# Kernel tuning notes

Hardware: AMD Instinct MI355X
Metric: run time of the kernel (lower is better)

Reference implementation:

```python
import jax, jax.numpy as jnp
import numpy as np

L, B, S, H = 2, 32, 2048, 512


def setup_inputs() -> dict:
    key = jax.random.key(0)
    k0, k1, k2, k3, k4 = jax.random.split(key, 5)
    scale = 1.0 / np.sqrt(H).astype(np.float32)  # ~PyTorch LSTMCell init scale
    return {
        "X": jax.random.normal(k0, (B, S, H), jnp.float32),
        "W_ih": jax.random.normal(k1, (L, 4 * H, H), jnp.float32) * scale,
        "W_hh": jax.random.normal(k2, (L, 4 * H, H), jnp.float32) * scale,
        "b_ih": jax.random.normal(k3, (L, 4 * H), jnp.float32) * scale,
        "b_hh": jax.random.normal(k4, (L, 4 * H), jnp.float32) * scale,
    }


def _lstm_layer(x, Wih, Whh, bih, bhh):
    # x: [S, B, I]; gate order matches torch.nn.LSTMCell: i, f, g, o
    Bb = x.shape[1]
    Hh = Whh.shape[1]
    h0 = jnp.zeros((Bb, Hh), x.dtype)
    c0 = jnp.zeros((Bb, Hh), x.dtype)
    # precompute input contribution for all timesteps: [S, B, 4H]
    xg = jnp.einsum('sbi,gi->sbg', x, Wih) + bih + bhh

    def step(carry, xg_t):
        h, c = carry
        gates = xg_t + h @ Whh.T  # [B, 4H]
        i, f, g, o = jnp.split(gates, 4, axis=-1)
        c = jax.nn.sigmoid(f) * c + jax.nn.sigmoid(i) * jnp.tanh(g)
        h = jax.nn.sigmoid(o) * jnp.tanh(c)
        return (h, c), h

    (hT, cT), hs = jax.lax.scan(step, (h0, c0), xg)
    return hs, hT, cT  # hs: [S, B, H]


def reference(X, W_ih, W_hh, b_ih, b_hh):
    # eval mode: variational dropout (dropout_i = dropout_h = 0) is identity;
    # no residual, no reverse.
    x = jnp.transpose(X, (1, 0, 2))  # [S, B, I]
    n_layers = W_ih.shape[0]
    hT = cT = None
    for l in range(n_layers):
        x, hT, cT = _lstm_layer(x, W_ih[l], W_hh[l], b_ih[l], b_hh[l])
    ht = jnp.transpose(x, (1, 0, 2))  # [B, S, H]
    # states = (ht[:, -1], ct[:, -1]) of final layer
    return ht, hT, cT
```

## Files before the change

kernel.cpp:

```cpp
#include <hip/hip_runtime.h>

typedef unsigned short u16;
typedef unsigned int u32;
typedef unsigned long long u64;
typedef __attribute__((ext_vector_type(4))) float f32x4;
typedef __attribute__((ext_vector_type(8))) short bf16x8;
typedef __attribute__((ext_vector_type(4))) u32 u32x4;

#define S_LEN 2048
#define BATCH 32
#define HID 512
#define NG 2048
#define NWG 64
#define SLICE 8

#define SENT 0x40004000u

#define MFMA16(a, b, c) __builtin_amdgcn_mfma_f32_16x16x32_bf16((a), (b), (c), 0, 0, 0)

__device__ __forceinline__ u16 f2bf(float f) {
  u32 u = __builtin_bit_cast(u32, f);
  u32 r = (u + 0x7FFFu + ((u >> 16) & 1u)) >> 16;
  return (u16)r;
}
__device__ __forceinline__ float bf2f(u16 u) {
  u32 x = ((u32)u) << 16;
  return __builtin_bit_cast(float, x);
}
__device__ __forceinline__ float sigf(float x) {
  return 1.0f / (1.0f + __expf(-x));
}
__device__ __forceinline__ float tanh_fast(float x) {
  float a = fabsf(x);
  float t = __expf(-2.0f * a);
  float r = (1.0f - t) / (1.0f + t);
  return x < 0.0f ? -r : r;
}

__device__ __forceinline__ u32x4 bypass_ld16(const u16* p) {
  u32x4 r;
  asm volatile("global_load_dwordx4 %0, %1, off sc0 sc1"
               : "=v"(r) : "v"(p) : "memory");
  return r;
}
__device__ __forceinline__ void bypass_st16(u16* p, u32x4 v) {
  asm volatile("global_store_dwordx4 %0, %1, off sc0 sc1"
               :: "v"(p), "v"(v) : "memory");
}
__device__ __forceinline__ void bypass_wait() {
  asm volatile("s_waitcnt vmcnt(0)" ::: "memory");
  __builtin_amdgcn_sched_barrier(0);
}

__global__ void fill_sentinel(u16* base, int n16) {
  u32x4 v = {SENT, SENT, SENT, SENT};
  const int step = gridDim.x * 256;
  for (int i = blockIdx.x * 256 + threadIdx.x; i < n16; i += step)
    bypass_st16(base + (size_t)i * 8, v);
  asm volatile("s_waitcnt vmcnt(0)" ::: "memory");
}

__global__ void prep_weights(const float* __restrict__ Wih, const float* __restrict__ Whh,
                             const float* __restrict__ bih, const float* __restrict__ bhh,
                             u16* __restrict__ wih_bf, u16* __restrict__ whh_bf,
                             float* __restrict__ bsum) {
  const int i = blockIdx.x * 256 + threadIdx.x;
  wih_bf[i] = f2bf(Wih[i]);
  whh_bf[i] = f2bf(Whh[i]);
  if (i < 2 * NG) bsum[i] = bih[i] + bhh[i];
}

__global__ __launch_bounds__(256)
void gemm_xg(const float* __restrict__ Ap, const u16* __restrict__ Bw,
             const float* __restrict__ bias, void* __restrict__ xgp, int xg32)
{
  __shared__ __align__(16) u16 aT[64][72];
  __shared__ __align__(16) u16 bT[64][72];
  const int tid = threadIdx.x;
  const int nb = blockIdx.x;
  const int mb = blockIdx.y;
  const int lane = tid & 63, wid = tid >> 6;
  const int mw = (wid & 1) * 32, nw = (wid >> 1) * 32;
  f32x4 acc[2][2] = {{{0.f,0.f,0.f,0.f},{0.f,0.f,0.f,0.f}},
                     {{0.f,0.f,0.f,0.f},{0.f,0.f,0.f,0.f}}};

  const int arow = tid >> 2;
  const int gm = mb * 64 + arow;
  const int t = gm >> 5, b = gm & 31;
  const size_t aoff = ((size_t)b * S_LEN + t) * HID;
  const size_t boff = (size_t)(nb * 64 + arow) * HID;
  const int c16 = (tid & 3) * 16;

  for (int kb = 0; kb < 8; ++kb) {
    const int k0 = kb * 64;
    {
      const float* src = Ap + aoff + k0 + c16;
      #pragma unroll
      for (int q = 0; q < 4; ++q) {
        const float4 v = ((const float4*)src)[q];
        ushort4 w4;
        w4.x = f2bf(v.x); w4.y = f2bf(v.y); w4.z = f2bf(v.z); w4.w = f2bf(v.w);
        *(ushort4*)&aT[arow][c16 + q * 4] = w4;
      }
    }
    {
      const uint4* src = (const uint4*)(Bw + boff + k0 + c16);
      const uint4 v0 = src[0], v1 = src[1];
      *(uint4*)&bT[arow][c16] = v0;
      *(uint4*)&bT[arow][c16 + 8] = v1;
    }
    __syncthreads();
    #pragma unroll
    for (int kk = 0; kk < 2; ++kk) {
      const int ko = kk * 32 + (lane >> 4) * 8;
      const bf16x8 a0 = *(const bf16x8*)&aT[mw +      (lane & 15)][ko];
      const bf16x8 a1 = *(const bf16x8*)&aT[mw + 16 + (lane & 15)][ko];
      const bf16x8 b0 = *(const bf16x8*)&bT[nw +      (lane & 15)][ko];
      const bf16x8 b1 = *(const bf16x8*)&bT[nw + 16 + (lane & 15)][ko];
      acc[0][0] = MFMA16(a0, b0, acc[0][0]);
      acc[0][1] = MFMA16(a0, b1, acc[0][1]);
      acc[1][0] = MFMA16(a1, b0, acc[1][0]);
      acc[1][1] = MFMA16(a1, b1, acc[1][1]);
    }
    __syncthreads();
  }
  const int col = lane & 15, rb = (lane >> 4) * 4;
  #pragma unroll
  for (int fm = 0; fm < 2; ++fm) {
    #pragma unroll
    for (int fn = 0; fn < 2; ++fn) {
      const int gn = nb * 64 + nw + fn * 16 + col;
      const float bv = bias[gn];
      #pragma unroll
      for (int r = 0; r < 4; ++r) {
        const size_t gmr = (size_t)(mb * 64 + mw + fm * 16 + rb + r);
        const float v = acc[fm][fn][r] + bv;
        if (xg32) ((float*)xgp)[gmr * NG + gn] = v;
        else      ((u16*)xgp)[gmr * NG + gn] = f2bf(v);
      }
    }
  }
}

__global__ __launch_bounds__(256, 1)
void lstm_fused(const void* __restrict__ xgp, int xg32,
                const u16* __restrict__ whh_bf, const u16* __restrict__ wih_bf,
                const float* __restrict__ bsum,
                u16* __restrict__ hb1, u16* __restrict__ hb2,
                float* __restrict__ dout)
{
  __shared__ __align__(16) u16 wR[32][520];
  __shared__ __align__(16) u16 wI[32][520];
  __shared__ __align__(16) u16 hA[32][520];
  __shared__ __align__(16) u16 hB[32][520];
  __shared__ float gT[32][33];

  const int blk = blockIdx.x;
  const int layer = blk >> 6;
  const int w = blk & 63;
  const int tid = threadIdx.x;
  const int lane = tid & 63, wid = tid >> 6;
  const int mw = (wid & 1) * 16, nw = (wid >> 1) * 16;
  const int b = tid >> 3, j = tid & 7;

  const u16* Whh = whh_bf + (size_t)layer * NG * HID;
  #pragma unroll
  for (int i = tid; i < 32 * 64; i += 256) {
    const int r = i >> 6, ch = i & 63;
    const int gnrow = (r >> 3) * HID + w * SLICE + (r & 7);
    *(uint4*)&wR[r][ch * 8] = *(const uint4*)&Whh[(size_t)gnrow * HID + ch * 8];
  }
  float bv[4] = {0.f, 0.f, 0.f, 0.f};
  if (layer == 1) {
    const u16* Wih2 = wih_bf + (size_t)NG * HID;
    #pragma unroll
    for (int i = tid; i < 32 * 64; i += 256) {
      const int r = i >> 6, ch = i & 63;
      const int gnrow = (r >> 3) * HID + w * SLICE + (r & 7);
      *(uint4*)&wI[r][ch * 8] = *(const uint4*)&Wih2[(size_t)gnrow * HID + ch * 8];
    }
    #pragma unroll
    for (int g = 0; g < 4; ++g) bv[g] = bsum[NG + g * HID + w * SLICE + j];
  }
  u16* hb_own = layer ? hb2 : hb1;
  float c = 0.0f;
  __syncthreads();

  for (int t = 0; t < S_LEN; ++t) {
    float xv[4];

    if (layer == 0) {
      if (xg32) {
        const float* x = (const float*)xgp + ((size_t)t * BATCH + b) * NG + w * SLICE + j;
        #pragma unroll
        for (int g = 0; g < 4; ++g) xv[g] = __builtin_nontemporal_load(&x[g * HID]);
      } else {
        const u16* x = (const u16*)xgp + ((size_t)t * BATCH + b) * NG + w * SLICE + j;
        #pragma unroll
        for (int g = 0; g < 4; ++g) xv[g] = bf2f(__builtin_nontemporal_load(&x[g * HID]));
      }
    } else {
      #pragma unroll
      for (int g = 0; g < 4; ++g) xv[g] = bv[g];
    }

    const u16* srcA = nullptr;
    const u16* srcB = nullptr;
    if (layer == 1) {
      srcA = hb1 + (size_t)t * (BATCH * HID);
      if (t > 0) srcB = hb2 + (size_t)(t - 1) * (BATCH * HID);
    } else if (t > 0) {
      srcA = hb1 + (size_t)(t - 1) * (BATCH * HID);
    }
    u32x4 vA[8], vB[8];
    if (srcA) {
      while (true) {
        #pragma unroll
        for (int ii = 0; ii < 8; ++ii) {
          const int i = tid + ii * 256, r = i >> 6, cc = i & 63;
          vA[ii] = bypass_ld16(srcA + (size_t)r * HID + cc * 8);
        }
        if (srcB) {
          #pragma unroll
          for (int ii = 0; ii < 8; ++ii) {
            const int i = tid + ii * 256, r = i >> 6, cc = i & 63;
            vB[ii] = bypass_ld16(srcB + (size_t)r * HID + cc * 8);
          }
        }
        bypass_wait();
        u32 bad = 0;
        #pragma unroll
        for (int ii = 0; ii < 8; ++ii)
          bad |= (u32)(vA[ii][0] == SENT) | (u32)(vA[ii][1] == SENT) |
                 (u32)(vA[ii][2] == SENT) | (u32)(vA[ii][3] == SENT);
        if (srcB) {
          #pragma unroll
          for (int ii = 0; ii < 8; ++ii)
            bad |= (u32)(vB[ii][0] == SENT) | (u32)(vB[ii][1] == SENT) |
                   (u32)(vB[ii][2] == SENT) | (u32)(vB[ii][3] == SENT);
        }
        if (__all((int)(bad == 0))) break;
      }
      #pragma unroll
      for (int ii = 0; ii < 8; ++ii) {
        const int i = tid + ii * 256, r = i >> 6, cc = i & 63;
        *(u32x4*)&hA[r][cc * 8] = vA[ii];
      }
      if (srcB) {
        #pragma unroll
        for (int ii = 0; ii < 8; ++ii) {
          const int i = tid + ii * 256, r = i >> 6, cc = i & 63;
          *(u32x4*)&hB[r][cc * 8] = vB[ii];
        }
      }
    }
    __syncthreads();

    f32x4 ac0 = {0.f,0.f,0.f,0.f}, ac1 = {0.f,0.f,0.f,0.f};
    if (layer == 1) {
      #pragma unroll
      for (int kt = 0; kt < 16; ++kt) {
        const int ko = kt * 32 + (lane >> 4) * 8;
        const bf16x8 a  = *(const bf16x8*)&hA[mw + (lane & 15)][ko];
        const bf16x8 bb = *(const bf16x8*)&wI[nw + (lane & 15)][ko];
        if (kt & 1) ac1 = MFMA16(a, bb, ac1); else ac0 = MFMA16(a, bb, ac0);
      }
      if (t > 0) {
        #pragma unroll
        for (int kt = 0; kt < 16; ++kt) {
          const int ko = kt * 32 + (lane >> 4) * 8;
          const bf16x8 a  = *(const bf16x8*)&hB[mw + (lane & 15)][ko];
          const bf16x8 bb = *(const bf16x8*)&wR[nw + (lane & 15)][ko];
          if (kt & 1) ac1 = MFMA16(a, bb, ac1); else ac0 = MFMA16(a, bb, ac0);
        }
      }
    } else if (t > 0) {
      #pragma unroll
      for (int kt = 0; kt < 16; ++kt) {
        const int ko = kt * 32 + (lane >> 4) * 8;
        const bf16x8 a  = *(const bf16x8*)&hA[mw + (lane & 15)][ko];
        const bf16x8 bb = *(const bf16x8*)&wR[nw + (lane & 15)][ko];
        if (kt & 1) ac1 = MFMA16(a, bb, ac1); else ac0 = MFMA16(a, bb, ac0);
      }
    }
    const f32x4 acc = ac0 + ac1;

    #pragma unroll
    for (int r = 0; r < 4; ++r)
      gT[mw + (lane >> 4) * 4 + r][nw + (lane & 15)] = acc[r];
    __syncthreads();

    float pre[4];
    #pragma unroll
    for (int g = 0; g < 4; ++g) pre[g] = xv[g] + gT[b][g * SLICE + j];

    const float gi = sigf(pre[0]);
    const float gf = sigf(pre[1]);
    const float gg = tanh_fast(pre[2]);
    const float go = sigf(pre[3]);
    c = gf * c + gi * gg;
    const float h = go * tanh_fast(c);

    {
      const u32 me  = (u32)f2bf(h);
      const u32 oth = (u32)__shfl_xor((int)me, 1);
      if ((j & 1) == 0) {
        u32* dst = (u32*)(hb_own + (size_t)t * (BATCH * HID) + b * HID + w * SLICE + j);
        asm volatile("global_store_dword %0, %1, off sc0 sc1"
                     :: "v"(dst), "v"(me | (oth << 16)) : "memory");
      }
    }
    if (layer == 1) {
      dout[((size_t)b * S_LEN + t) * HID + w * SLICE + j] = h;
      if (t == S_LEN - 1) {
        dout[(size_t)BATCH * S_LEN * HID + b * HID + w * SLICE + j] = h;
        dout[(size_t)BATCH * S_LEN * HID + (size_t)BATCH * HID + b * HID + w * SLICE + j] = c;
      }
    }
  }
}

extern "C" void kernel_launch(void* const* d_in, const int* in_sizes, int n_in,
                              void* d_out, int out_size, void* d_ws, size_t ws_size,
                              hipStream_t stream) {
  (void)in_sizes; (void)n_in; (void)out_size;
  const float* X   = (const float*)d_in[0];
  const float* Wih = (const float*)d_in[1];
  const float* Whh = (const float*)d_in[2];
  const float* bih = (const float*)d_in[3];
  const float* bhh = (const float*)d_in[4];

  const size_t M      = (size_t)S_LEN * BATCH;
  const size_t xg_b32 = M * NG * 4;
  const size_t xg_b16 = M * NG * 2;
  const size_t hb_b   = M * HID * 2;
  const size_t w_b    = 2ull * NG * HID * 2;
  const size_t fixed  = 2 * hb_b + 2 * w_b + 16384 + 1024;

  const int xg32 = (ws_size >= xg_b32 + fixed) ? 1 : 0;

  char* p = (char*)d_ws;
  auto carve = [&](size_t bytes) { char* q = p; p += (bytes + 255) & ~(size_t)255; return q; };
  void* xg     = carve(xg32 ? xg_b32 : xg_b16);
  u16*  hb1    = (u16*)carve(hb_b);
  u16*  hb2    = (u16*)carve(hb_b);
  u16*  wih_bf = (u16*)carve(w_b);
  u16*  whh_bf = (u16*)carve(w_b);
  float* bsum  = (float*)carve(16384);

  fill_sentinel<<<2048, 256, 0, stream>>>(hb1, (int)((2 * hb_b) / 16));
  prep_weights<<<(2 * NG * HID) / 256, 256, 0, stream>>>(Wih, Whh, bih, bhh,
                                                         wih_bf, whh_bf, bsum);
  gemm_xg<<<dim3(32, 1024), 256, 0, stream>>>(X, wih_bf, bsum, xg, xg32);
  lstm_fused<<<2 * NWG, 256, 0, stream>>>(xg, xg32, whh_bf, wih_bf, bsum,
                                          hb1, hb2, (float*)d_out);
}
```

Measured before the change: 7.892 ms.

## Fuse both LSTM layers into one workgroup per slice with register-resident weights

```diff
diff --git a/kernel.cpp b/kernel.cpp
--- a/kernel.cpp
+++ b/kernel.cpp
@@ -149,47 +149,44 @@
                 u16* __restrict__ hb1, u16* __restrict__ hb2,
                 float* __restrict__ dout)
 {
-  __shared__ __align__(16) u16 wR[32][520];
-  __shared__ __align__(16) u16 wI[32][520];
   __shared__ __align__(16) u16 hA[32][520];
   __shared__ __align__(16) u16 hB[32][520];
-  __shared__ float gT[32][33];
-
-  const int blk = blockIdx.x;
-  const int layer = blk >> 6;
-  const int w = blk & 63;
+  __shared__ float gT1[32][33];
+  __shared__ float gT2[32][33];
+
+  const int w = blockIdx.x;
   const int tid = threadIdx.x;
   const int lane = tid & 63, wid = tid >> 6;
   const int mw = (wid & 1) * 16, nw = (wid >> 1) * 16;
   const int b = tid >> 3, j = tid & 7;
 
-  const u16* Whh = whh_bf + (size_t)layer * NG * HID;
+  bf16x8 w1f[16], wIf[16], w2f[16];
+  {
+    const int lrow = nw + (lane & 15);
+    const size_t gnrow = (size_t)(lrow >> 3) * HID + w * SLICE + (lrow & 7);
+    const u16* W1 = whh_bf + gnrow * HID;
+    const u16* WI = wih_bf + (size_t)NG * HID + gnrow * HID;
+    const u16* W2 = whh_bf + (size_t)NG * HID + gnrow * HID;
+    #pragma unroll
+    for (int kt = 0; kt < 16; ++kt) {
+      const int ko = kt * 32 + (lane >> 4) * 8;
+      w1f[kt] = *(const bf16x8*)&W1[ko];
+      wIf[kt] = *(const bf16x8*)&WI[ko];
+      w2f[kt] = *(const bf16x8*)&W2[ko];
+    }
+  }
+  float bv[4];
   #pragma unroll
-  for (int i = tid; i < 32 * 64; i += 256) {
-    const int r = i >> 6, ch = i & 63;
-    const int gnrow = (r >> 3) * HID + w * SLICE + (r & 7);
-    *(uint4*)&wR[r][ch * 8] = *(const uint4*)&Whh[(size_t)gnrow * HID + ch * 8];
-  }
-  float bv[4] = {0.f, 0.f, 0.f, 0.f};
-  if (layer == 1) {
-    const u16* Wih2 = wih_bf + (size_t)NG * HID;
-    #pragma unroll
-    for (int i = tid; i < 32 * 64; i += 256) {
-      const int r = i >> 6, ch = i & 63;
-      const int gnrow = (r >> 3) * HID + w * SLICE + (r & 7);
-      *(uint4*)&wI[r][ch * 8] = *(const uint4*)&Wih2[(size_t)gnrow * HID + ch * 8];
-    }
-    #pragma unroll
-    for (int g = 0; g < 4; ++g) bv[g] = bsum[NG + g * HID + w * SLICE + j];
-  }
-  u16* hb_own = layer ? hb2 : hb1;
-  float c = 0.0f;
+  for (int g = 0; g < 4; ++g) bv[g] = bsum[NG + g * HID + w * SLICE + j];
+
+  float c1 = 0.0f, c2 = 0.0f;
   __syncthreads();
 
-  for (int t = 0; t < S_LEN; ++t) {
-    float xv[4];
-
-    if (layer == 0) {
+  for (int t = 0; t <= S_LEN; ++t) {
+    const int u = t - 1;
+    float xv[4] = {0.f, 0.f, 0.f, 0.f};
+
+    if (t < S_LEN) {
       if (xg32) {
         const float* x = (const float*)xgp + ((size_t)t * BATCH + b) * NG + w * SLICE + j;
         #pragma unroll
@@ -199,21 +196,12 @@
         #pragma unroll
         for (int g = 0; g < 4; ++g) xv[g] = bf2f(__builtin_nontemporal_load(&x[g * HID]));
       }
-    } else {
-      #pragma unroll
-      for (int g = 0; g < 4; ++g) xv[g] = bv[g];
-    }
-
-    const u16* srcA = nullptr;
-    const u16* srcB = nullptr;
-    if (layer == 1) {
-      srcA = hb1 + (size_t)t * (BATCH * HID);
-      if (t > 0) srcB = hb2 + (size_t)(t - 1) * (BATCH * HID);
-    } else if (t > 0) {
-      srcA = hb1 + (size_t)(t - 1) * (BATCH * HID);
-    }
-    u32x4 vA[8], vB[8];
-    if (srcA) {
+    }
+
+    if (t >= 1) {
+      const u16* srcA = hb1 + (size_t)(t - 1) * (BATCH * HID);
+      const u16* srcB = (t >= 2) ? hb2 + (size_t)(t - 2) * (BATCH * HID) : nullptr;
+      u32x4 vA[8], vB[8];
       while (true) {
         #pragma unroll
         for (int ii = 0; ii < 8; ++ii) {
@@ -256,65 +244,84 @@
     }
     __syncthreads();
 
-    f32x4 ac0 = {0.f,0.f,0.f,0.f}, ac1 = {0.f,0.f,0.f,0.f};
-    if (layer == 1) {
+    f32x4 ac1a = {0.f,0.f,0.f,0.f}, ac1b = {0.f,0.f,0.f,0.f};
+    f32x4 ac2a = {0.f,0.f,0.f,0.f}, ac2b = {0.f,0.f,0.f,0.f};
+    if (t >= 1) {
+      bf16x8 af[16];
       #pragma unroll
       for (int kt = 0; kt < 16; ++kt) {
         const int ko = kt * 32 + (lane >> 4) * 8;
-        const bf16x8 a  = *(const bf16x8*)&hA[mw + (lane & 15)][ko];
-        const bf16x8 bb = *(const bf16x8*)&wI[nw + (lane & 15)][ko];
-        if (kt & 1) ac1 = MFMA16(a, bb, ac1); else ac0 = MFMA16(a, bb, ac0);
-      }
-      if (t > 0) {
+        af[kt] = *(const bf16x8*)&hA[mw + (lane & 15)][ko];
+      }
+      if (t < S_LEN) {
+        #pragma unroll
+        for (int kt = 0; kt < 16; ++kt) {
+          if (kt & 1) ac1b = MFMA16(af[kt], w1f[kt], ac1b);
+          else        ac1a = MFMA16(af[kt], w1f[kt], ac1a);
+        }
+      }
+      #pragma unroll
+      for (int kt = 0; kt < 16; ++kt)
+        ac2a = MFMA16(af[kt], wIf[kt], ac2a);
+      if (t >= 2) {
         #pragma unroll
         for (int kt = 0; kt < 16; ++kt) {
           const int ko = kt * 32 + (lane >> 4) * 8;
-          const bf16x8 a  = *(const bf16x8*)&hB[mw + (lane & 15)][ko];
-          const bf16x8 bb = *(const bf16x8*)&wR[nw + (lane & 15)][ko];
-          if (kt & 1) ac1 = MFMA16(a, bb, ac1); else ac0 = MFMA16(a, bb, ac0);
-        }
-      }
-    } else if (t > 0) {
-      #pragma unroll
-      for (int kt = 0; kt < 16; ++kt) {
-        const int ko = kt * 32 + (lane >> 4) * 8;
-        const bf16x8 a  = *(const bf16x8*)&hA[mw + (lane & 15)][ko];
-        const bf16x8 bb = *(const bf16x8*)&wR[nw + (lane & 15)][ko];
-        if (kt & 1) ac1 = MFMA16(a, bb, ac1); else ac0 = MFMA16(a, bb, ac0);
-      }
-    }
-    const f32x4 acc = ac0 + ac1;
+          const bf16x8 bfr = *(const bf16x8*)&hB[mw + (lane & 15)][ko];
+          ac2b = MFMA16(bfr, w2f[kt], ac2b);
+        }
+      }
+    }
+    const f32x4 acc1 = ac1a + ac1b;
+    const f32x4 acc2 = ac2a + ac2b;
 
     #pragma unroll
-    for (int r = 0; r < 4; ++r)
-      gT[mw + (lane >> 4) * 4 + r][nw + (lane & 15)] = acc[r];
+    for (int r = 0; r < 4; ++r) {
+      gT1[mw + (lane >> 4) * 4 + r][nw + (lane & 15)] = acc1[r];
+      gT2[mw + (lane >> 4) * 4 + r][nw + (lane & 15)] = acc2[r];
+    }
     __syncthreads();
 
-    float pre[4];
-    #pragma unroll
-    for (int g = 0; g < 4; ++g) pre[g] = xv[g] + gT[b][g * SLICE + j];
-
-    const float gi = sigf(pre[0]);
-    const float gf = sigf(pre[1]);
-    const float gg = tanh_fast(pre[2]);
-    const float go = sigf(pre[3]);
-    c = gf * c + gi * gg;
-    const float h = go * tanh_fast(c);
-
-    {
+    if (t < S_LEN) {
+      float pre[4];
+      #pragma unroll
+      for (int g = 0; g < 4; ++g) pre[g] = xv[g] + gT1[b][g * SLICE + j];
+      const float gi = sigf(pre[0]);
+      const float gf = sigf(pre[1]);
+      const float gg = tanh_fast(pre[2]);
+      const float go = sigf(pre[3]);
+      c1 = gf * c1 + gi * gg;
+      const float h = go * tanh_fast(c1);
       const u32 me  = (u32)f2bf(h);
       const u32 oth = (u32)__shfl_xor((int)me, 1);
       if ((j & 1) == 0) {
-        u32* dst = (u32*)(hb_own + (size_t)t * (BATCH * HID) + b * HID + w * SLICE + j);
+        u32* dst = (u32*)(hb1 + (size_t)t * (BATCH * HID) + b * HID + w * SLICE + j);
         asm volatile("global_store_dword %0, %1, off sc0 sc1"
                      :: "v"(dst), "v"(me | (oth << 16)) : "memory");
       }
     }
-    if (layer == 1) {
-      dout[((size_t)b * S_LEN + t) * HID + w * SLICE + j] = h;
-      if (t == S_LEN - 1) {
+
+    if (t >= 1) {
+      float pre[4];
+      #pragma unroll
+      for (int g = 0; g < 4; ++g) pre[g] = bv[g] + gT2[b][g * SLICE + j];
+      const float gi = sigf(pre[0]);
+      const float gf = sigf(pre[1]);
+      const float gg = tanh_fast(pre[2]);
+      const float go = sigf(pre[3]);
+      c2 = gf * c2 + gi * gg;
+      const float h = go * tanh_fast(c2);
+      const u32 me  = (u32)f2bf(h);
+      const u32 oth = (u32)__shfl_xor((int)me, 1);
+      if ((j & 1) == 0) {
+        u32* dst = (u32*)(hb2 + (size_t)u * (BATCH * HID) + b * HID + w * SLICE + j);
+        asm volatile("global_store_dword %0, %1, off sc0 sc1"
+                     :: "v"(dst), "v"(me | (oth << 16)) : "memory");
+      }
+      dout[((size_t)b * S_LEN + u) * HID + w * SLICE + j] = h;
+      if (u == S_LEN - 1) {
         dout[(size_t)BATCH * S_LEN * HID + b * HID + w * SLICE + j] = h;
-        dout[(size_t)BATCH * S_LEN * HID + (size_t)BATCH * HID + b * HID + w * SLICE + j] = c;
+        dout[(size_t)BATCH * S_LEN * HID + (size_t)BATCH * HID + b * HID + w * SLICE + j] = c2;
       }
     }
   }
@@ -352,6 +359,6 @@
   prep_weights<<<(2 * NG * HID) / 256, 256, 0, stream>>>(Wih, Whh, bih, bhh,
                                                          wih_bf, whh_bf, bsum);
   gemm_xg<<<dim3(32, 1024), 256, 0, stream>>>(X, wih_bf, bsum, xg, xg32);
-  lstm_fused<<<2 * NWG, 256, 0, stream>>>(xg, xg32, whh_bf, wih_bf, bsum,
-                                          hb1, hb2, (float*)d_out);
-}
+  lstm_fused<<<NWG, 256, 0, stream>>>(xg, xg32, whh_bf, wih_bf, bsum,
+                                      hb1, hb2, (float*)d_out);
+}
```

Result: slower. 10.68 ms (+35.3%).
